# Optimization experiments

Hardware: AMD Instinct MI355X
Metric: run time of the kernel (lower is better)

## Reference

```python
import jax, jax.numpy as jnp
import numpy as np

EMBED = 1024
HEADS = 16
HEAD_DIM = EMBED // HEADS
FF = 4 * EMBED
B, S = 2, 2048


def setup_inputs() -> dict:
    key = jax.random.key(0)
    ks = jax.random.split(key, 16)
    sd = 0.02
    inp = {
        "x": jax.random.normal(ks[0], (B, S, EMBED), dtype=jnp.float32),
        "Wq": jax.random.normal(ks[1], (EMBED, EMBED), dtype=jnp.float32) * sd,
        "bq": jnp.zeros((EMBED,), jnp.float32),
        "Wk": jax.random.normal(ks[2], (EMBED, EMBED), dtype=jnp.float32) * sd,
        "bk": jnp.zeros((EMBED,), jnp.float32),
        "Wv": jax.random.normal(ks[3], (EMBED, EMBED), dtype=jnp.float32) * sd,
        "bv": jnp.zeros((EMBED,), jnp.float32),
        "Wo": jax.random.normal(ks[4], (EMBED, EMBED), dtype=jnp.float32) * sd,
        "W1": jax.random.normal(ks[5], (EMBED, FF), dtype=jnp.float32) * sd,
        "b1": jnp.zeros((FF,), jnp.float32),
        "W2": jax.random.normal(ks[6], (FF, EMBED), dtype=jnp.float32) * sd,
        "b2": jnp.zeros((EMBED,), jnp.float32),
        "g1": jnp.ones((EMBED,), jnp.float32),
        "be1": jnp.zeros((EMBED,), jnp.float32),
        "g2": jnp.ones((EMBED,), jnp.float32),
        "be2": jnp.zeros((EMBED,), jnp.float32),
    }
    return inp


def _layernorm(x, g, b, eps=1e-5):
    mu = jnp.mean(x, axis=-1, keepdims=True)
    var = jnp.mean(jnp.square(x - mu), axis=-1, keepdims=True)
    return (x - mu) * jax.lax.rsqrt(var + eps) * g + b


def _attn(x, Wq, bq, Wk, bk, Wv, bv, Wo):
    b, s, d = x.shape
    q = (x @ Wq + bq).reshape(b, s, HEADS, HEAD_DIM)
    k = (x @ Wk + bk).reshape(b, s, HEADS, HEAD_DIM)
    v = (x @ Wv + bv).reshape(b, s, HEADS, HEAD_DIM)
    # NOTE: original scales by sqrt(embed_dim), NOT sqrt(head_dim)
    logits = jnp.einsum('bqhd,bkhd->bhqk', q, k) / jnp.sqrt(jnp.float32(d))
    mask = jnp.tril(jnp.ones((s, s), dtype=bool))
    logits = jnp.where(mask, logits, -jnp.inf)
    w = jax.nn.softmax(logits, axis=-1)
    z = jnp.einsum('bhqk,bkhd->bqhd', w, v).reshape(b, s, d)
    return z @ Wo


def reference(x, Wq, bq, Wk, bk, Wv, bv, Wo, W1, b1, W2, b2, g1, be1, g2, be2):
    h = x + _attn(_layernorm(x, g1, be1), Wq, bq, Wk, bk, Wv, bv, Wo)
    m = _layernorm(h, g2, be2)
    m = jax.nn.gelu(m @ W1 + b1, approximate=False) @ W2 + b2
    return h + m
```

## Files before the change

### kernel.cpp

```cpp
#include <hip/hip_runtime.h>
#include <cstdint>
#include <cstddef>
#include <math.h>

#define EMBED 1024
#define SEQ   2048
#define NROWS 4096
#define NHEADS 16

typedef __bf16 bf16x8 __attribute__((ext_vector_type(8)));
typedef float f32x4 __attribute__((ext_vector_type(4)));
typedef unsigned short us8 __attribute__((ext_vector_type(8)));
typedef unsigned short us4 __attribute__((ext_vector_type(4)));

__device__ __forceinline__ unsigned short f2bf(float f) {
  union { float f; unsigned u; } v; v.f = f;
  unsigned r = v.u + 0x7fffu + ((v.u >> 16) & 1u);
  return (unsigned short)(r >> 16);
}
__device__ __forceinline__ float bf2f(unsigned short u) {
  union { unsigned u; float f; } v; v.u = (unsigned)u << 16; return v.f;
}

__device__ __forceinline__ bf16x8 as_bf(us8 u) { return __builtin_bit_cast(bf16x8, u); }

__global__ __launch_bounds__(256) void transpose_all(
    const float* __restrict__ Wq, const float* __restrict__ Wk,
    const float* __restrict__ Wv, const float* __restrict__ Wo,
    const float* __restrict__ W1, const float* __restrict__ W2,
    unsigned short* __restrict__ wqT, unsigned short* __restrict__ wkT,
    unsigned short* __restrict__ wvT, unsigned short* __restrict__ woT,
    unsigned short* __restrict__ w1T, unsigned short* __restrict__ w2T) {
  __shared__ float tile[32][33];
  const int bid = blockIdx.x;
  const float* in;
  unsigned short* out;
  int K, N, bx, by;
  if (bid < 4096) {
    const int w = bid >> 10, t = bid & 1023;
    in  = (w == 0) ? Wq  : (w == 1) ? Wk  : (w == 2) ? Wv  : Wo;
    out = (w == 0) ? wqT : (w == 1) ? wkT : (w == 2) ? wvT : woT;
    K = 1024; N = 1024; bx = t & 31; by = t >> 5;
  } else if (bid < 8192) {
    const int t = bid - 4096;
    in = W1; out = w1T; K = 1024; N = 4096; bx = t & 127; by = t >> 7;
  } else {
    const int t = bid - 8192;
    in = W2; out = w2T; K = 4096; N = 1024; bx = t & 31; by = t >> 5;
  }
  const int tx = threadIdx.x & 31, ty = threadIdx.x >> 5;
  const int n0 = bx * 32, k0 = by * 32;
#pragma unroll
  for (int i = 0; i < 4; i++) {
    int k = ty + i * 8;
    tile[k][tx] = in[(size_t)(k0 + k) * N + n0 + tx];
  }
  __syncthreads();
#pragma unroll
  for (int i = 0; i < 4; i++) {
    int n = ty + i * 8;
    out[(size_t)(n0 + n) * K + k0 + tx] = f2bf(tile[tx][n]);
  }
}

__global__ __launch_bounds__(256) void layernorm_bf16(
    const float* __restrict__ x, const float* __restrict__ g,
    const float* __restrict__ be, unsigned short* __restrict__ out) {
  const int wave = threadIdx.x >> 6, lane = threadIdx.x & 63;
  const int row = blockIdx.x * 4 + wave;
  const float* xr = x + (size_t)row * EMBED;
  float4 v[4];
  float s = 0.f, sq = 0.f;
#pragma unroll
  for (int c = 0; c < 4; c++) {
    v[c] = *(const float4*)&xr[c * 256 + lane * 4];
    s  += v[c].x + v[c].y + v[c].z + v[c].w;
    sq += v[c].x * v[c].x + v[c].y * v[c].y + v[c].z * v[c].z + v[c].w * v[c].w;
  }
#pragma unroll
  for (int m = 1; m < 64; m <<= 1) {
    s  += __shfl_xor(s, m, 64);
    sq += __shfl_xor(sq, m, 64);
  }
  const float mean = s * (1.f / 1024.f);
  const float var  = sq * (1.f / 1024.f) - mean * mean;
  const float rstd = rsqrtf(var + 1e-5f);
#pragma unroll
  for (int c = 0; c < 4; c++) {
    const int idx = c * 256 + lane * 4;
    us4 o;
    o[0] = f2bf((v[c].x - mean) * rstd * g[idx + 0] + be[idx + 0]);
    o[1] = f2bf((v[c].y - mean) * rstd * g[idx + 1] + be[idx + 1]);
    o[2] = f2bf((v[c].z - mean) * rstd * g[idx + 2] + be[idx + 2]);
    o[3] = f2bf((v[c].w - mean) * rstd * g[idx + 3] + be[idx + 3]);
    *(us4*)&out[(size_t)row * EMBED + idx] = o;
  }
}

__global__ __launch_bounds__(256) void ln2_fused(
    const float* __restrict__ x,
    const unsigned short* __restrict__ pw0,
    const unsigned short* __restrict__ pw1,
    const float* __restrict__ g, const float* __restrict__ be,
    float* __restrict__ hb, unsigned short* __restrict__ out) {
  const int wave = threadIdx.x >> 6, lane = threadIdx.x & 63;
  const int row = blockIdx.x * 4 + wave;
  const size_t rb = (size_t)row * EMBED;
  float4 v[4];
  float s = 0.f, sq = 0.f;
#pragma unroll
  for (int c = 0; c < 4; c++) {
    const int idx = c * 256 + lane * 4;
    const float4 xv = *(const float4*)&x[rb + idx];
    const us4 a = *(const us4*)&pw0[rb + idx];
    const us4 d = *(const us4*)&pw1[rb + idx];
    v[c].x = xv.x + bf2f(a[0]) + bf2f(d[0]);
    v[c].y = xv.y + bf2f(a[1]) + bf2f(d[1]);
    v[c].z = xv.z + bf2f(a[2]) + bf2f(d[2]);
    v[c].w = xv.w + bf2f(a[3]) + bf2f(d[3]);
    *(float4*)&hb[rb + idx] = v[c];
    s  += v[c].x + v[c].y + v[c].z + v[c].w;
    sq += v[c].x * v[c].x + v[c].y * v[c].y + v[c].z * v[c].z + v[c].w * v[c].w;
  }
#pragma unroll
  for (int m = 1; m < 64; m <<= 1) {
    s  += __shfl_xor(s, m, 64);
    sq += __shfl_xor(sq, m, 64);
  }
  const float mean = s * (1.f / 1024.f);
  const float var  = sq * (1.f / 1024.f) - mean * mean;
  const float rstd = rsqrtf(var + 1e-5f);
#pragma unroll
  for (int c = 0; c < 4; c++) {
    const int idx = c * 256 + lane * 4;
    us4 o;
    o[0] = f2bf((v[c].x - mean) * rstd * g[idx + 0] + be[idx + 0]);
    o[1] = f2bf((v[c].y - mean) * rstd * g[idx + 1] + be[idx + 1]);
    o[2] = f2bf((v[c].z - mean) * rstd * g[idx + 2] + be[idx + 2]);
    o[3] = f2bf((v[c].w - mean) * rstd * g[idx + 3] + be[idx + 3]);
    *(us4*)&out[rb + idx] = o;
  }
}

enum { MODE_QKV = 0, MODE_WO = 1, MODE_FF1 = 2, MODE_FF2 = 3, MODE_PART = 4 };

#define LDW 36

template <int MODE, int NITER>
__global__ __launch_bounds__(256) void gemm_bf16(
    const unsigned short* __restrict__ A,
    const unsigned short* __restrict__ Bt0,
    const unsigned short* __restrict__ Bt1,
    const unsigned short* __restrict__ Bt2,
    const float* __restrict__ bias0,
    const float* __restrict__ bias1,
    const float* __restrict__ bias2,
    const float* __restrict__ res,
    void* __restrict__ out0, void* __restrict__ out1,
    void* __restrict__ out2, void* __restrict__ out3,
    int M, int N, int K) {
  const unsigned short* Bt = Bt0;
  const float* bias = bias0;
  void* outv = out0;
  int zidx = 0;
  if constexpr (MODE == MODE_QKV) {
    zidx = blockIdx.z;
    if (zidx == 1)      { Bt = Bt1; bias = bias1; outv = out1; }
    else if (zidx == 2) { Bt = Bt2; bias = bias2; outv = out2; }
  }
  if constexpr (MODE == MODE_PART) {
    zidx = blockIdx.z;
    outv = (zidx == 0) ? out0 : (zidx == 1) ? out1 : (zidx == 2) ? out2 : out3;
  }
  const int koff = (MODE == MODE_PART) ? zidx * (NITER * 32) : 0;

  __shared__ unsigned short As[2][128 * LDW];
  __shared__ unsigned short Bs[2][128 * LDW];
  const int tid = threadIdx.x;
  const int wave = tid >> 6, lane = tid & 63;
  const int quad = lane >> 4, l15 = lane & 15;
  const int wr = (wave >> 1) * 64, wc = (wave & 1) * 64;
  const int rowA0 = blockIdx.y * 128, colB0 = blockIdx.x * 128;

  const int srow = tid >> 2;
  const int scol = (tid & 3) * 8;
  const unsigned short* gA = A  + (size_t)(rowA0 + srow) * K + koff + scol;
  const unsigned short* gB = Bt + (size_t)(colB0 + srow) * K + koff + scol;
  const size_t half = (size_t)64 * K;

  us8 pa0[3], pa1[3], pb0[3], pb1[3];
#pragma unroll
  for (int s = 0; s < 3; s++) {
    if (s < NITER) {
      pa0[s] = *(const us8*)(gA + s * 32);
      pa1[s] = *(const us8*)(gA + half + s * 32);
      pb0[s] = *(const us8*)(gB + s * 32);
      pb1[s] = *(const us8*)(gB + half + s * 32);
    }
  }
  *(us8*)&As[0][srow * LDW + scol]        = pa0[0];
  *(us8*)&As[0][(srow + 64) * LDW + scol] = pa1[0];
  *(us8*)&Bs[0][srow * LDW + scol]        = pb0[0];
  *(us8*)&Bs[0][(srow + 64) * LDW + scol] = pb1[0];
  __syncthreads();

  f32x4 acc[4][4];
#pragma unroll
  for (int i = 0; i < 4; i++)
#pragma unroll
    for (int j = 0; j < 4; j++) acc[i][j] = f32x4{0.f, 0.f, 0.f, 0.f};

#pragma unroll
  for (int k = 0; k < NITER; k++) {
    const int buf = k & 1;
    if (k + 1 < NITER) {
      const int s = (k + 1) % 3;
      *(us8*)&As[buf ^ 1][srow * LDW + scol]        = pa0[s];
      *(us8*)&As[buf ^ 1][(srow + 64) * LDW + scol] = pa1[s];
      *(us8*)&Bs[buf ^ 1][srow * LDW + scol]        = pb0[s];
      *(us8*)&Bs[buf ^ 1][(srow + 64) * LDW + scol] = pb1[s];
    }
    if (k + 3 < NITER) {
      const int s = k % 3;
      pa0[s] = *(const us8*)(gA + (size_t)(k + 3) * 32);
      pa1[s] = *(const us8*)(gA + half + (size_t)(k + 3) * 32);
      pb0[s] = *(const us8*)(gB + (size_t)(k + 3) * 32);
      pb1[s] = *(const us8*)(gB + half + (size_t)(k + 3) * 32);
    }
    bf16x8 af[4], bfr[4];
#pragma unroll
    for (int mi = 0; mi < 4; mi++)
      af[mi] = as_bf(*(const us8*)&As[buf][(wr + mi * 16 + l15) * LDW + quad * 8]);
#pragma unroll
    for (int ni = 0; ni < 4; ni++)
      bfr[ni] = as_bf(*(const us8*)&Bs[buf][(wc + ni * 16 + l15) * LDW + quad * 8]);
#pragma unroll
    for (int mi = 0; mi < 4; mi++)
#pragma unroll
      for (int ni = 0; ni < 4; ni++)
        acc[mi][ni] = __builtin_amdgcn_mfma_f32_16x16x32_bf16(af[mi], bfr[ni], acc[mi][ni], 0, 0, 0);
    if (k + 1 < NITER) __syncthreads();
  }

#pragma unroll
  for (int ni = 0; ni < 4; ni++) {
    const int col = colB0 + wc + ni * 16 + l15;
    float bv = 0.f;
    if constexpr (MODE == MODE_QKV || MODE == MODE_FF1 || MODE == MODE_FF2) bv = bias[col];
#pragma unroll
    for (int mi = 0; mi < 4; mi++) {
      const int row0 = rowA0 + wr + mi * 16 + quad * 4;
      if constexpr (MODE == MODE_QKV) {
        unsigned short* o = (unsigned short*)outv;
        if (zidx == 2) {
          us4 pk;
#pragma unroll
          for (int r = 0; r < 4; r++) pk[r] = f2bf(acc[mi][ni][r] + bv);
          const int bb = row0 >> 11;
          const int sr = row0 & 2047;
          *(us4*)&o[((size_t)(bb * 1024 + col)) * SEQ + sr] = pk;
        } else {
#pragma unroll
          for (int r = 0; r < 4; r++)
            o[(size_t)(row0 + r) * N + col] = f2bf(acc[mi][ni][r] + bv);
        }
      } else if constexpr (MODE == MODE_FF1) {
        unsigned short* o = (unsigned short*)outv;
#pragma unroll
        for (int r = 0; r < 4; r++) {
          float v = acc[mi][ni][r] + bv;
          v = 0.5f * v * (1.f + erff(v * 0.7071067811865476f));
          o[(size_t)(row0 + r) * N + col] = f2bf(v);
        }
      } else if constexpr (MODE == MODE_PART) {
        unsigned short* o = (unsigned short*)outv;
#pragma unroll
        for (int r = 0; r < 4; r++)
          o[(size_t)(row0 + r) * N + col] = f2bf(acc[mi][ni][r]);
      } else {
        float* o = (float*)outv;
#pragma unroll
        for (int r = 0; r < 4; r++) {
          float v = acc[mi][ni][r] + bv + res[(size_t)(row0 + r) * N + col];
          o[(size_t)(row0 + r) * N + col] = v;
        }
      }
    }
  }
}

__global__ __launch_bounds__(256) void ff2_reduce(
    const float* __restrict__ hb, const float* __restrict__ b2,
    const unsigned short* __restrict__ p0, const unsigned short* __restrict__ p1,
    const unsigned short* __restrict__ p2, const unsigned short* __restrict__ p3,
    float* __restrict__ out) {
  const size_t i = ((size_t)blockIdx.x * 256 + threadIdx.x) * 4;
  const int col = (int)(i & (EMBED - 1));
  const float4 h = *(const float4*)&hb[i];
  const float4 bb = *(const float4*)&b2[col];
  const us4 a = *(const us4*)&p0[i];
  const us4 b = *(const us4*)&p1[i];
  const us4 c = *(const us4*)&p2[i];
  const us4 d = *(const us4*)&p3[i];
  float4 o;
  o.x = h.x + bb.x + bf2f(a[0]) + bf2f(b[0]) + bf2f(c[0]) + bf2f(d[0]);
  o.y = h.y + bb.y + bf2f(a[1]) + bf2f(b[1]) + bf2f(c[1]) + bf2f(d[1]);
  o.z = h.z + bb.z + bf2f(a[2]) + bf2f(b[2]) + bf2f(c[2]) + bf2f(d[2]);
  o.w = h.w + bb.w + bf2f(a[3]) + bf2f(b[3]) + bf2f(c[3]) + bf2f(d[3]);
  *(float4*)&out[i] = o;
}

__global__ __launch_bounds__(256) void attn_kernel(
    const unsigned short* __restrict__ Q,
    const unsigned short* __restrict__ Kb,
    const unsigned short* __restrict__ Vt,
    unsigned short* __restrict__ Z) {
  __shared__ unsigned short Ksh[64][72];
  __shared__ unsigned short Vsh[64][72];
  __shared__ unsigned short Pt[4][16][72];
  __shared__ float Ot[4][64][17];

  const int tid = threadIdx.x;
  const int wave = tid >> 6, lane = tid & 63;
  const int quad = lane >> 4, l15 = lane & 15;
  const int bh = blockIdx.x, b = bh >> 4, h = bh & 15;
  const float cscale = 1.4426950408889634f / 32.f;

  const int srow = tid >> 2;
  const int sc = (tid & 3) * 8;
  const unsigned short* Kbase = Kb + (size_t)(b * SEQ) * EMBED + h * 64;
  const unsigned short* Vbase = Vt + (size_t)(b * 1024 + h * 64) * SEQ;

#pragma unroll
  for (int ph = 0; ph < 2; ph++) {
    const int j = ph ? 31 - (int)blockIdx.y : (int)blockIdx.y;
    const int qc = j * 64 + wave * 16;

    bf16x8 qf[2];
#pragma unroll
    for (int kf = 0; kf < 2; kf++)
      qf[kf] = as_bf(*(const us8*)&Q[(size_t)(b * SEQ + qc + l15) * EMBED +
                                     h * 64 + kf * 32 + quad * 8]);

    f32x4 accO[4];
#pragma unroll
    for (int dt = 0; dt < 4; dt++) accO[dt] = f32x4{0.f, 0.f, 0.f, 0.f};
    float mrun = -INFINITY, lrun = 0.f;

    for (int kt = 0; kt <= j; kt++) {
      const int kbase = kt * 64;
      const unsigned short* kg = Kbase + (size_t)(kbase + srow) * EMBED + sc;
      const unsigned short* vg = Vbase + (size_t)srow * SEQ + kbase + sc;
      const us8 k0 = *(const us8*)kg;
      const us8 k1 = *(const us8*)(kg + 32);
      const us8 v0 = *(const us8*)vg;
      const us8 v1 = *(const us8*)(vg + 32);
      __syncthreads();
      *(us8*)&Ksh[srow][sc]      = k0;
      *(us8*)&Ksh[srow][32 + sc] = k1;
      *(us8*)&Vsh[srow][sc]      = v0;
      *(us8*)&Vsh[srow][32 + sc] = v1;
      __syncthreads();

      f32x4 sf[4];
#pragma unroll
      for (int nt = 0; nt < 4; nt++) {
        f32x4 z4 = f32x4{0.f, 0.f, 0.f, 0.f};
#pragma unroll
        for (int kf = 0; kf < 2; kf++) {
          const bf16x8 ka = as_bf(*(const us8*)&Ksh[nt * 16 + l15][kf * 32 + quad * 8]);
          z4 = __builtin_amdgcn_mfma_f32_16x16x32_bf16(ka, qf[kf], z4, 0, 0, 0);
        }
        sf[nt] = z4 * cscale;
      }
      if (kt == j) {
        const int q = qc + l15;
#pragma unroll
        for (int nt = 0; nt < 4; nt++) {
          const int key0 = kbase + nt * 16 + quad * 4;
#pragma unroll
          for (int r = 0; r < 4; r++)
            if (key0 + r > q) sf[nt][r] = -INFINITY;
        }
      }
      float mx = sf[0][0];
#pragma unroll
      for (int nt = 0; nt < 4; nt++)
#pragma unroll
        for (int r = 0; r < 4; r++) mx = fmaxf(mx, sf[nt][r]);
      mx = fmaxf(mx, __shfl_xor(mx, 16, 64));
      mx = fmaxf(mx, __shfl_xor(mx, 32, 64));
      const float mnew = fmaxf(mrun, mx);
      const float alpha = exp2f(mrun - mnew);
      mrun = mnew;
      float rs = 0.f;
#pragma unroll
      for (int nt = 0; nt < 4; nt++) {
        us4 pk;
#pragma unroll
        for (int r = 0; r < 4; r++) {
          const float p = exp2f(sf[nt][r] - mnew);
          rs += p;
          pk[r] = f2bf(p);
        }
        *(us4*)&Pt[wave][l15][nt * 16 + quad * 4] = pk;
      }
      rs += __shfl_xor(rs, 16, 64);
      rs += __shfl_xor(rs, 32, 64);
      lrun = lrun * alpha + rs;
#pragma unroll
      for (int dt = 0; dt < 4; dt++) accO[dt] = accO[dt] * alpha;
      bf16x8 pf[2];
#pragma unroll
      for (int kk = 0; kk < 2; kk++)
        pf[kk] = as_bf(*(const us8*)&Pt[wave][l15][kk * 32 + quad * 8]);
#pragma unroll
      for (int dt = 0; dt < 4; dt++)
#pragma unroll
        for (int kk = 0; kk < 2; kk++) {
          const bf16x8 va = as_bf(*(const us8*)&Vsh[dt * 16 + l15][kk * 32 + quad * 8]);
          accO[dt] = __builtin_amdgcn_mfma_f32_16x16x32_bf16(va, pf[kk], accO[dt], 0, 0, 0);
        }
    }

    const float inv = 1.f / lrun;
#pragma unroll
    for (int dt = 0; dt < 4; dt++)
#pragma unroll
      for (int r = 0; r < 4; r++)
        Ot[wave][dt * 16 + quad * 4 + r][l15] = accO[dt][r] * inv;
    const int lq = lane >> 2, dbase = (lane & 3) * 16;
    us8 o0, o1;
#pragma unroll
    for (int i = 0; i < 8; i++) o0[i] = f2bf(Ot[wave][dbase + i][lq]);
#pragma unroll
    for (int i = 0; i < 8; i++) o1[i] = f2bf(Ot[wave][dbase + 8 + i][lq]);
    unsigned short* zp = Z + (size_t)(b * SEQ + qc + lq) * EMBED + h * 64 + dbase;
    *(us8*)zp = o0;
    *(us8*)(zp + 8) = o1;
  }
}

extern "C" void kernel_launch(void* const* d_in, const int* in_sizes, int n_in,
                              void* d_out, int out_size, void* d_ws, size_t ws_size,
                              hipStream_t stream) {
  const float* x   = (const float*)d_in[0];
  const float* Wq  = (const float*)d_in[1];
  const float* bq  = (const float*)d_in[2];
  const float* Wk  = (const float*)d_in[3];
  const float* bk  = (const float*)d_in[4];
  const float* Wv  = (const float*)d_in[5];
  const float* bv  = (const float*)d_in[6];
  const float* Wo  = (const float*)d_in[7];
  const float* W1  = (const float*)d_in[8];
  const float* b1  = (const float*)d_in[9];
  const float* W2  = (const float*)d_in[10];
  const float* b2  = (const float*)d_in[11];
  const float* g1  = (const float*)d_in[12];
  const float* be1 = (const float*)d_in[13];
  const float* g2  = (const float*)d_in[14];
  const float* be2 = (const float*)d_in[15];
  float* out = (float*)d_out;

  char* ws = (char*)d_ws;
  const size_t MB = 1024 * 1024;
  unsigned short* wqT = (unsigned short*)(ws + 0 * MB);
  unsigned short* wkT = (unsigned short*)(ws + 2 * MB);
  unsigned short* wvT = (unsigned short*)(ws + 4 * MB);
  unsigned short* woT = (unsigned short*)(ws + 6 * MB);
  unsigned short* w1T = (unsigned short*)(ws + 8 * MB);
  unsigned short* w2T = (unsigned short*)(ws + 16 * MB);
  unsigned short* ln1 = (unsigned short*)(ws + 24 * MB);
  unsigned short* zb  = (unsigned short*)(ws + 24 * MB);
  unsigned short* ln2 = (unsigned short*)(ws + 24 * MB);
  unsigned short* p2  = (unsigned short*)(ws + 24 * MB);
  unsigned short* qb  = (unsigned short*)(ws + 32 * MB);
  unsigned short* kb2 = (unsigned short*)(ws + 40 * MB);
  float*          hb  = (float*)         (ws + 32 * MB);
  unsigned short* vT  = (unsigned short*)(ws + 48 * MB);
  unsigned short* pw0 = (unsigned short*)(ws + 48 * MB);
  unsigned short* p3  = (unsigned short*)(ws + 48 * MB);
  unsigned short* pw1 = (unsigned short*)(ws + 56 * MB);
  unsigned short* m1  = (unsigned short*)(ws + 56 * MB);
  unsigned short* p0  = (unsigned short*)(ws + 0 * MB);
  unsigned short* p1  = (unsigned short*)(ws + 8 * MB);
  (void)in_sizes; (void)n_in; (void)out_size; (void)ws_size;

  transpose_all<<<12288, 256, 0, stream>>>(Wq, Wk, Wv, Wo, W1, W2,
                                           wqT, wkT, wvT, woT, w1T, w2T);

  layernorm_bf16<<<NROWS / 4, 256, 0, stream>>>(x, g1, be1, ln1);

  gemm_bf16<MODE_QKV, 32><<<dim3(8, 32, 3), 256, 0, stream>>>(
      ln1, wqT, wkT, wvT, bq, bk, bv, nullptr, qb, kb2, vT, nullptr,
      NROWS, 1024, 1024);

  attn_kernel<<<dim3(32, 16), 256, 0, stream>>>(qb, kb2, vT, zb);

  gemm_bf16<MODE_PART, 16><<<dim3(8, 32, 2), 256, 0, stream>>>(
      zb, woT, nullptr, nullptr, nullptr, nullptr, nullptr, nullptr,
      pw0, pw1, nullptr, nullptr, NROWS, 1024, 1024);

  ln2_fused<<<NROWS / 4, 256, 0, stream>>>(x, pw0, pw1, g2, be2, hb, ln2);

  gemm_bf16<MODE_FF1, 32><<<dim3(32, 32), 256, 0, stream>>>(
      ln2, w1T, nullptr, nullptr, b1, nullptr, nullptr, nullptr,
      m1, nullptr, nullptr, nullptr, NROWS, 4096, 1024);

  gemm_bf16<MODE_PART, 32><<<dim3(8, 32, 4), 256, 0, stream>>>(
      m1, w2T, nullptr, nullptr, nullptr, nullptr, nullptr, nullptr,
      p0, p1, p2, p3, NROWS, 1024, 4096);

  ff2_reduce<<<NROWS * EMBED / (256 * 4), 256, 0, stream>>>(
      hb, b2, p0, p1, p2, p3, out);
}
```

Baseline: 379.0 us.

## Load GEMM MFMA fragments directly from global memory, dropping LDS staging

```diff
diff --git a/kernel.cpp b/kernel.cpp
--- a/kernel.cpp
+++ b/kernel.cpp
@@ -144,10 +144,8 @@
 
 enum { MODE_QKV = 0, MODE_WO = 1, MODE_FF1 = 2, MODE_FF2 = 3, MODE_PART = 4 };
 
-#define LDW 36
-
 template <int MODE, int NITER>
-__global__ __launch_bounds__(256) void gemm_bf16(
+__global__ __launch_bounds__(256, 2) void gemm_bf16(
     const unsigned short* __restrict__ A,
     const unsigned short* __restrict__ Bt0,
     const unsigned short* __restrict__ Bt1,
@@ -174,72 +172,49 @@
   }
   const int koff = (MODE == MODE_PART) ? zidx * (NITER * 32) : 0;
 
-  __shared__ unsigned short As[2][128 * LDW];
-  __shared__ unsigned short Bs[2][128 * LDW];
   const int tid = threadIdx.x;
   const int wave = tid >> 6, lane = tid & 63;
   const int quad = lane >> 4, l15 = lane & 15;
   const int wr = (wave >> 1) * 64, wc = (wave & 1) * 64;
   const int rowA0 = blockIdx.y * 128, colB0 = blockIdx.x * 128;
 
-  const int srow = tid >> 2;
-  const int scol = (tid & 3) * 8;
-  const unsigned short* gA = A  + (size_t)(rowA0 + srow) * K + koff + scol;
-  const unsigned short* gB = Bt + (size_t)(colB0 + srow) * K + koff + scol;
-  const size_t half = (size_t)64 * K;
-
-  us8 pa0[3], pa1[3], pb0[3], pb1[3];
-#pragma unroll
-  for (int s = 0; s < 3; s++) {
-    if (s < NITER) {
-      pa0[s] = *(const us8*)(gA + s * 32);
-      pa1[s] = *(const us8*)(gA + half + s * 32);
-      pb0[s] = *(const us8*)(gB + s * 32);
-      pb1[s] = *(const us8*)(gB + half + s * 32);
+  const unsigned short* pA[4];
+  const unsigned short* pB[4];
+#pragma unroll
+  for (int t = 0; t < 4; t++) {
+    pA[t] = A  + (size_t)(rowA0 + wr + t * 16 + l15) * K + koff + quad * 8;
+    pB[t] = Bt + (size_t)(colB0 + wc + t * 16 + l15) * K + koff + quad * 8;
+  }
+
+  f32x4 acc[4][4];
+#pragma unroll
+  for (int i = 0; i < 4; i++)
+#pragma unroll
+    for (int j = 0; j < 4; j++) acc[i][j] = f32x4{0.f, 0.f, 0.f, 0.f};
+
+  us8 fa[2][4], fb[2][4];
+#pragma unroll
+  for (int t = 0; t < 4; t++) {
+    fa[0][t] = *(const us8*)pA[t];
+    fb[0][t] = *(const us8*)pB[t];
+  }
+
+#pragma unroll
+  for (int k = 0; k < NITER; k++) {
+    const int cur = k & 1;
+    if (k + 1 < NITER) {
+#pragma unroll
+      for (int t = 0; t < 4; t++) {
+        fa[cur ^ 1][t] = *(const us8*)(pA[t] + (k + 1) * 32);
+        fb[cur ^ 1][t] = *(const us8*)(pB[t] + (k + 1) * 32);
+      }
     }
-  }
-  *(us8*)&As[0][srow * LDW + scol]        = pa0[0];
-  *(us8*)&As[0][(srow + 64) * LDW + scol] = pa1[0];
-  *(us8*)&Bs[0][srow * LDW + scol]        = pb0[0];
-  *(us8*)&Bs[0][(srow + 64) * LDW + scol] = pb1[0];
-  __syncthreads();
-
-  f32x4 acc[4][4];
-#pragma unroll
-  for (int i = 0; i < 4; i++)
-#pragma unroll
-    for (int j = 0; j < 4; j++) acc[i][j] = f32x4{0.f, 0.f, 0.f, 0.f};
-
-#pragma unroll
-  for (int k = 0; k < NITER; k++) {
-    const int buf = k & 1;
-    if (k + 1 < NITER) {
-      const int s = (k + 1) % 3;
-      *(us8*)&As[buf ^ 1][srow * LDW + scol]        = pa0[s];
-      *(us8*)&As[buf ^ 1][(srow + 64) * LDW + scol] = pa1[s];
-      *(us8*)&Bs[buf ^ 1][srow * LDW + scol]        = pb0[s];
-      *(us8*)&Bs[buf ^ 1][(srow + 64) * LDW + scol] = pb1[s];
-    }
-    if (k + 3 < NITER) {
-      const int s = k % 3;
-      pa0[s] = *(const us8*)(gA + (size_t)(k + 3) * 32);
-      pa1[s] = *(const us8*)(gA + half + (size_t)(k + 3) * 32);
-      pb0[s] = *(const us8*)(gB + (size_t)(k + 3) * 32);
-      pb1[s] = *(const us8*)(gB + half + (size_t)(k + 3) * 32);
-    }
-    bf16x8 af[4], bfr[4];
 #pragma unroll
     for (int mi = 0; mi < 4; mi++)
-      af[mi] = as_bf(*(const us8*)&As[buf][(wr + mi * 16 + l15) * LDW + quad * 8]);
-#pragma unroll
-    for (int ni = 0; ni < 4; ni++)
-      bfr[ni] = as_bf(*(const us8*)&Bs[buf][(wc + ni * 16 + l15) * LDW + quad * 8]);
-#pragma unroll
-    for (int mi = 0; mi < 4; mi++)
 #pragma unroll
       for (int ni = 0; ni < 4; ni++)
-        acc[mi][ni] = __builtin_amdgcn_mfma_f32_16x16x32_bf16(af[mi], bfr[ni], acc[mi][ni], 0, 0, 0);
-    if (k + 1 < NITER) __syncthreads();
+        acc[mi][ni] = __builtin_amdgcn_mfma_f32_16x16x32_bf16(
+            as_bf(fa[cur][mi]), as_bf(fb[cur][ni]), acc[mi][ni], 0, 0, 0);
   }
 
 #pragma unroll
```

Measured after the change: 662.0 us. 1.75x slower.

## Add 128x256-tile GEMM for FFN layers and merge layernorm into prep kernel

Applied to the files above, without the earlier changes.

```diff
diff --git a/kernel.cpp b/kernel.cpp
--- a/kernel.cpp
+++ b/kernel.cpp
@@ -24,76 +24,76 @@
 
 __device__ __forceinline__ bf16x8 as_bf(us8 u) { return __builtin_bit_cast(bf16x8, u); }
 
-__global__ __launch_bounds__(256) void transpose_all(
+__global__ __launch_bounds__(256) void prep_kernel(
     const float* __restrict__ Wq, const float* __restrict__ Wk,
     const float* __restrict__ Wv, const float* __restrict__ Wo,
     const float* __restrict__ W1, const float* __restrict__ W2,
     unsigned short* __restrict__ wqT, unsigned short* __restrict__ wkT,
     unsigned short* __restrict__ wvT, unsigned short* __restrict__ woT,
-    unsigned short* __restrict__ w1T, unsigned short* __restrict__ w2T) {
+    unsigned short* __restrict__ w1T, unsigned short* __restrict__ w2T,
+    const float* __restrict__ x, const float* __restrict__ g1,
+    const float* __restrict__ be1, unsigned short* __restrict__ ln1) {
   __shared__ float tile[32][33];
   const int bid = blockIdx.x;
-  const float* in;
-  unsigned short* out;
-  int K, N, bx, by;
-  if (bid < 4096) {
-    const int w = bid >> 10, t = bid & 1023;
-    in  = (w == 0) ? Wq  : (w == 1) ? Wk  : (w == 2) ? Wv  : Wo;
-    out = (w == 0) ? wqT : (w == 1) ? wkT : (w == 2) ? wvT : woT;
-    K = 1024; N = 1024; bx = t & 31; by = t >> 5;
-  } else if (bid < 8192) {
-    const int t = bid - 4096;
-    in = W1; out = w1T; K = 1024; N = 4096; bx = t & 127; by = t >> 7;
+  if (bid < 12288) {
+    const float* in;
+    unsigned short* out;
+    int K, N, bx, by;
+    if (bid < 4096) {
+      const int w = bid >> 10, t = bid & 1023;
+      in  = (w == 0) ? Wq  : (w == 1) ? Wk  : (w == 2) ? Wv  : Wo;
+      out = (w == 0) ? wqT : (w == 1) ? wkT : (w == 2) ? wvT : woT;
+      K = 1024; N = 1024; bx = t & 31; by = t >> 5;
+    } else if (bid < 8192) {
+      const int t = bid - 4096;
+      in = W1; out = w1T; K = 1024; N = 4096; bx = t & 127; by = t >> 7;
+    } else {
+      const int t = bid - 8192;
+      in = W2; out = w2T; K = 4096; N = 1024; bx = t & 31; by = t >> 5;
+    }
+    const int tx = threadIdx.x & 31, ty = threadIdx.x >> 5;
+    const int n0 = bx * 32, k0 = by * 32;
+#pragma unroll
+    for (int i = 0; i < 4; i++) {
+      int k = ty + i * 8;
+      tile[k][tx] = in[(size_t)(k0 + k) * N + n0 + tx];
+    }
+    __syncthreads();
+#pragma unroll
+    for (int i = 0; i < 4; i++) {
+      int n = ty + i * 8;
+      out[(size_t)(n0 + n) * K + k0 + tx] = f2bf(tile[tx][n]);
+    }
   } else {
-    const int t = bid - 8192;
-    in = W2; out = w2T; K = 4096; N = 1024; bx = t & 31; by = t >> 5;
-  }
-  const int tx = threadIdx.x & 31, ty = threadIdx.x >> 5;
-  const int n0 = bx * 32, k0 = by * 32;
-#pragma unroll
-  for (int i = 0; i < 4; i++) {
-    int k = ty + i * 8;
-    tile[k][tx] = in[(size_t)(k0 + k) * N + n0 + tx];
-  }
-  __syncthreads();
-#pragma unroll
-  for (int i = 0; i < 4; i++) {
-    int n = ty + i * 8;
-    out[(size_t)(n0 + n) * K + k0 + tx] = f2bf(tile[tx][n]);
-  }
-}
-
-__global__ __launch_bounds__(256) void layernorm_bf16(
-    const float* __restrict__ x, const float* __restrict__ g,
-    const float* __restrict__ be, unsigned short* __restrict__ out) {
-  const int wave = threadIdx.x >> 6, lane = threadIdx.x & 63;
-  const int row = blockIdx.x * 4 + wave;
-  const float* xr = x + (size_t)row * EMBED;
-  float4 v[4];
-  float s = 0.f, sq = 0.f;
-#pragma unroll
-  for (int c = 0; c < 4; c++) {
-    v[c] = *(const float4*)&xr[c * 256 + lane * 4];
-    s  += v[c].x + v[c].y + v[c].z + v[c].w;
-    sq += v[c].x * v[c].x + v[c].y * v[c].y + v[c].z * v[c].z + v[c].w * v[c].w;
-  }
-#pragma unroll
-  for (int m = 1; m < 64; m <<= 1) {
-    s  += __shfl_xor(s, m, 64);
-    sq += __shfl_xor(sq, m, 64);
-  }
-  const float mean = s * (1.f / 1024.f);
-  const float var  = sq * (1.f / 1024.f) - mean * mean;
-  const float rstd = rsqrtf(var + 1e-5f);
-#pragma unroll
-  for (int c = 0; c < 4; c++) {
-    const int idx = c * 256 + lane * 4;
-    us4 o;
-    o[0] = f2bf((v[c].x - mean) * rstd * g[idx + 0] + be[idx + 0]);
-    o[1] = f2bf((v[c].y - mean) * rstd * g[idx + 1] + be[idx + 1]);
-    o[2] = f2bf((v[c].z - mean) * rstd * g[idx + 2] + be[idx + 2]);
-    o[3] = f2bf((v[c].w - mean) * rstd * g[idx + 3] + be[idx + 3]);
-    *(us4*)&out[(size_t)row * EMBED + idx] = o;
+    const int wave = threadIdx.x >> 6, lane = threadIdx.x & 63;
+    const int row = (bid - 12288) * 4 + wave;
+    const float* xr = x + (size_t)row * EMBED;
+    float4 v[4];
+    float s = 0.f, sq = 0.f;
+#pragma unroll
+    for (int c = 0; c < 4; c++) {
+      v[c] = *(const float4*)&xr[c * 256 + lane * 4];
+      s  += v[c].x + v[c].y + v[c].z + v[c].w;
+      sq += v[c].x * v[c].x + v[c].y * v[c].y + v[c].z * v[c].z + v[c].w * v[c].w;
+    }
+#pragma unroll
+    for (int m = 1; m < 64; m <<= 1) {
+      s  += __shfl_xor(s, m, 64);
+      sq += __shfl_xor(sq, m, 64);
+    }
+    const float mean = s * (1.f / 1024.f);
+    const float var  = sq * (1.f / 1024.f) - mean * mean;
+    const float rstd = rsqrtf(var + 1e-5f);
+#pragma unroll
+    for (int c = 0; c < 4; c++) {
+      const int idx = c * 256 + lane * 4;
+      us4 o;
+      o[0] = f2bf((v[c].x - mean) * rstd * g1[idx + 0] + be1[idx + 0]);
+      o[1] = f2bf((v[c].y - mean) * rstd * g1[idx + 1] + be1[idx + 1]);
+      o[2] = f2bf((v[c].z - mean) * rstd * g1[idx + 2] + be1[idx + 2]);
+      o[3] = f2bf((v[c].w - mean) * rstd * g1[idx + 3] + be1[idx + 3]);
+      *(us4*)&ln1[(size_t)row * EMBED + idx] = o;
+    }
   }
 }
 
@@ -264,7 +264,124 @@
           for (int r = 0; r < 4; r++)
             o[(size_t)(row0 + r) * N + col] = f2bf(acc[mi][ni][r] + bv);
         }
-      } else if constexpr (MODE == MODE_FF1) {
+      } else if constexpr (MODE == MODE_PART) {
+        unsigned short* o = (unsigned short*)outv;
+#pragma unroll
+        for (int r = 0; r < 4; r++)
+          o[(size_t)(row0 + r) * N + col] = f2bf(acc[mi][ni][r]);
+      } else {
+        float* o = (float*)outv;
+#pragma unroll
+        for (int r = 0; r < 4; r++) {
+          float v = acc[mi][ni][r] + bv + res[(size_t)(row0 + r) * N + col];
+          o[(size_t)(row0 + r) * N + col] = v;
+        }
+      }
+    }
+  }
+}
+
+template <int MODE, int NITER>
+__global__ __launch_bounds__(256, 2) void gemm_big(
+    const unsigned short* __restrict__ A,
+    const unsigned short* __restrict__ Bt,
+    const float* __restrict__ bias,
+    void* __restrict__ out0, void* __restrict__ out1,
+    void* __restrict__ out2, void* __restrict__ out3,
+    int M, int N, int K) {
+  void* outv = out0;
+  int zidx = 0;
+  if constexpr (MODE == MODE_PART) {
+    zidx = blockIdx.z;
+    outv = (zidx == 0) ? out0 : (zidx == 1) ? out1 : (zidx == 2) ? out2 : out3;
+  }
+  const int koff = (MODE == MODE_PART) ? zidx * (NITER * 32) : 0;
+
+  __shared__ unsigned short As[2][128 * LDW];
+  __shared__ unsigned short Bs[2][256 * LDW];
+  const int tid = threadIdx.x;
+  const int wave = tid >> 6, lane = tid & 63;
+  const int quad = lane >> 4, l15 = lane & 15;
+  const int wr = (wave >> 1) * 64;
+  const int wc = (wave & 1) * 128;
+  const int rowA0 = blockIdx.y * 128, colB0 = blockIdx.x * 256;
+
+  const int srow = tid >> 2;
+  const int scol = (tid & 3) * 8;
+  const unsigned short* gA = A  + (size_t)(rowA0 + srow) * K + koff + scol;
+  const unsigned short* gB = Bt + (size_t)(colB0 + srow) * K + koff + scol;
+  const size_t h64 = (size_t)64 * K;
+
+  us8 pa[2][2], pb[2][4];
+#pragma unroll
+  for (int s = 0; s < 2; s++) {
+    pa[s][0] = *(const us8*)(gA + s * 32);
+    pa[s][1] = *(const us8*)(gA + h64 + s * 32);
+#pragma unroll
+    for (int j = 0; j < 4; j++)
+      pb[s][j] = *(const us8*)(gB + (size_t)j * h64 + s * 32);
+  }
+  *(us8*)&As[0][srow * LDW + scol]        = pa[0][0];
+  *(us8*)&As[0][(srow + 64) * LDW + scol] = pa[0][1];
+#pragma unroll
+  for (int j = 0; j < 4; j++)
+    *(us8*)&Bs[0][(srow + 64 * j) * LDW + scol] = pa[0][0][0] == pa[0][0][0] ? pb[0][j] : pb[0][j];
+  if (2 < NITER) {
+    pa[0][0] = *(const us8*)(gA + 2 * 32);
+    pa[0][1] = *(const us8*)(gA + h64 + 2 * 32);
+#pragma unroll
+    for (int j = 0; j < 4; j++)
+      pb[0][j] = *(const us8*)(gB + (size_t)j * h64 + 2 * 32);
+  }
+  __syncthreads();
+
+  f32x4 acc[4][8];
+#pragma unroll
+  for (int i = 0; i < 4; i++)
+#pragma unroll
+    for (int j = 0; j < 8; j++) acc[i][j] = f32x4{0.f, 0.f, 0.f, 0.f};
+
+#pragma unroll
+  for (int k = 0; k < NITER; k++) {
+    const int buf = k & 1;
+    if (k + 1 < NITER) {
+      const int s = (k + 1) & 1;
+      *(us8*)&As[buf ^ 1][srow * LDW + scol]        = pa[s][0];
+      *(us8*)&As[buf ^ 1][(srow + 64) * LDW + scol] = pa[s][1];
+#pragma unroll
+      for (int j = 0; j < 4; j++)
+        *(us8*)&Bs[buf ^ 1][(srow + 64 * j) * LDW + scol] = pb[s][j];
+      if (k + 3 < NITER) {
+        pa[s][0] = *(const us8*)(gA + (size_t)(k + 3) * 32);
+        pa[s][1] = *(const us8*)(gA + h64 + (size_t)(k + 3) * 32);
+#pragma unroll
+        for (int j = 0; j < 4; j++)
+          pb[s][j] = *(const us8*)(gB + (size_t)j * h64 + (size_t)(k + 3) * 32);
+      }
+    }
+    bf16x8 af[4];
+#pragma unroll
+    for (int mi = 0; mi < 4; mi++)
+      af[mi] = as_bf(*(const us8*)&As[buf][(wr + mi * 16 + l15) * LDW + quad * 8]);
+#pragma unroll
+    for (int ni = 0; ni < 8; ni++) {
+      const bf16x8 bfr = as_bf(*(const us8*)&Bs[buf][(wc + ni * 16 + l15) * LDW + quad * 8]);
+#pragma unroll
+      for (int mi = 0; mi < 4; mi++)
+        acc[mi][ni] = __builtin_amdgcn_mfma_f32_16x16x32_bf16(af[mi], bfr, acc[mi][ni], 0, 0, 0);
+    }
+    if (k + 1 < NITER) __syncthreads();
+  }
+
+#pragma unroll
+  for (int ni = 0; ni < 8; ni++) {
+    const int col = colB0 + wc + ni * 16 + l15;
+    float bv = 0.f;
+    if constexpr (MODE == MODE_FF1) bv = bias[col];
+#pragma unroll
+    for (int mi = 0; mi < 4; mi++) {
+      const int row0 = rowA0 + wr + mi * 16 + quad * 4;
+      if constexpr (MODE == MODE_FF1) {
         unsigned short* o = (unsigned short*)outv;
 #pragma unroll
         for (int r = 0; r < 4; r++) {
@@ -272,18 +389,11 @@
           v = 0.5f * v * (1.f + erff(v * 0.7071067811865476f));
           o[(size_t)(row0 + r) * N + col] = f2bf(v);
         }
-      } else if constexpr (MODE == MODE_PART) {
+      } else {
         unsigned short* o = (unsigned short*)outv;
 #pragma unroll
         for (int r = 0; r < 4; r++)
           o[(size_t)(row0 + r) * N + col] = f2bf(acc[mi][ni][r]);
-      } else {
-        float* o = (float*)outv;
-#pragma unroll
-        for (int r = 0; r < 4; r++) {
-          float v = acc[mi][ni][r] + bv + res[(size_t)(row0 + r) * N + col];
-          o[(size_t)(row0 + r) * N + col] = v;
-        }
       }
     }
   }
@@ -486,10 +596,8 @@
   unsigned short* p1  = (unsigned short*)(ws + 8 * MB);
   (void)in_sizes; (void)n_in; (void)out_size; (void)ws_size;
 
-  transpose_all<<<12288, 256, 0, stream>>>(Wq, Wk, Wv, Wo, W1, W2,
-                                           wqT, wkT, wvT, woT, w1T, w2T);
-
-  layernorm_bf16<<<NROWS / 4, 256, 0, stream>>>(x, g1, be1, ln1);
+  prep_kernel<<<12288 + NROWS / 4, 256, 0, stream>>>(
+      Wq, Wk, Wv, Wo, W1, W2, wqT, wkT, wvT, woT, w1T, w2T, x, g1, be1, ln1);
 
   gemm_bf16<MODE_QKV, 32><<<dim3(8, 32, 3), 256, 0, stream>>>(
       ln1, wqT, wkT, wvT, bq, bk, bv, nullptr, qb, kb2, vT, nullptr,
@@ -503,13 +611,11 @@
 
   ln2_fused<<<NROWS / 4, 256, 0, stream>>>(x, pw0, pw1, g2, be2, hb, ln2);
 
-  gemm_bf16<MODE_FF1, 32><<<dim3(32, 32), 256, 0, stream>>>(
-      ln2, w1T, nullptr, nullptr, b1, nullptr, nullptr, nullptr,
-      m1, nullptr, nullptr, nullptr, NROWS, 4096, 1024);
-
-  gemm_bf16<MODE_PART, 32><<<dim3(8, 32, 4), 256, 0, stream>>>(
-      m1, w2T, nullptr, nullptr, nullptr, nullptr, nullptr, nullptr,
-      p0, p1, p2, p3, NROWS, 1024, 4096);
+  gemm_big<MODE_FF1, 32><<<dim3(16, 32), 256, 0, stream>>>(
+      ln2, w1T, b1, m1, nullptr, nullptr, nullptr, NROWS, 4096, 1024);
+
+  gemm_big<MODE_PART, 32><<<dim3(4, 32, 4), 256, 0, stream>>>(
+      m1, w2T, nullptr, p0, p1, p2, p3, NROWS, 1024, 4096);
 
   ff2_reduce<<<NROWS * EMBED / (256 * 4), 256, 0, stream>>>(
       hb, b2, p0, p1, p2, p3, out);
```

Measured after the change: 369.7 us. 1.03x faster.
